# Optimization experiments

Hardware: AMD Instinct MI355X
Metric: run time of the kernel (lower is better)

The kernel has to match this reference:

```python
import jax, jax.numpy as jnp
import numpy as np

T, B, D, R = 1024, 32, 1024, 128

def _orth_cols(key, n, r):
    # mimic torch QR-based orthogonal init: Q[:, :r] of a random [n, r] matrix
    a = jax.random.normal(key, (n, r), dtype=jnp.float32)
    q, _ = jnp.linalg.qr(a)
    return q[:, :r]

def setup_inputs() -> dict:
    key = jax.random.key(0)
    ks = jax.random.split(key, 8)
    x = jax.random.normal(ks[0], (T, B, D), dtype=jnp.float32)
    z = jax.random.normal(ks[1], (T, B, D), dtype=jnp.float32)
    h0 = jnp.zeros((B, D), dtype=jnp.float32)
    U_h = _orth_cols(ks[2], D, R)
    V_h = _orth_cols(ks[3], D, R).T  # [R, D] with orthonormal rows
    U_x = _orth_cols(ks[4], D, R)
    V_x = _orth_cols(ks[5], D, R).T
    s_h = jnp.ones((R,), dtype=jnp.float32)
    s_x = jnp.ones((R,), dtype=jnp.float32)
    b = jnp.zeros((D,), dtype=jnp.float32)
    return {"x": x, "z": z, "h0": h0, "U_h": U_h, "V_h": V_h, "s_h": s_h,
            "U_x": U_x, "V_x": V_x, "s_x": s_x, "b": b}

def reference(x, z, h0, U_h, V_h, s_h, U_x, V_x, s_x, b):
    # Precompute V_x @ x_t for all timesteps: [T, B, R]
    Vx_all = jnp.einsum('tbd,rd->tbr', x, V_x)
    Ux_all = jnp.einsum('tbr,dr->tbd', s_x * Vx_all, U_x)  # input branch, no recurrence

    def step(h_prev, inp):
        Ux_t, z_t = inp
        Vh = h_prev @ V_h.T                 # [B, R]
        Uh = (s_h * Vh) @ U_h.T             # [B, D]
        h_new = jnp.tanh(Uh + Ux_t + b)
        out_t = h_new * jax.nn.silu(z_t)
        return h_new, (h_new, out_t)

    _, (hs, output) = jax.lax.scan(step, h0, (Ux_all, z))
    h = jnp.concatenate([h0[None], hs], axis=0)  # [T+1, B, D]
    return output, h
```

## Files before the change

### kernel.cpp

```cpp
#include <hip/hip_runtime.h>
#include <cstdint>

#define T_STEPS 1024
#define BATCH   32
#define DIM     1024
#define RANK    128
#define BD      (BATCH*DIM)
#define TBD     ((size_t)T_STEPS*BD)

typedef _Float16 half2v __attribute__((ext_vector_type(2)));

__device__ __forceinline__ float dot2f(uint32_t a, uint32_t b, float acc) {
#if __has_builtin(__builtin_amdgcn_fdot2)
  return __builtin_amdgcn_fdot2(__builtin_bit_cast(half2v, a),
                                __builtin_bit_cast(half2v, b), acc, false);
#else
  half2v xx = __builtin_bit_cast(half2v, a);
  half2v yy = __builtin_bit_cast(half2v, b);
  return acc + (float)xx[0]*(float)yy[0] + (float)xx[1]*(float)yy[1];
#endif
}

__device__ __forceinline__ float dot2x4(uint4 w, uint4 h, float acc) {
  acc = dot2f(w.x, h.x, acc); acc = dot2f(w.y, h.y, acc);
  acc = dot2f(w.z, h.z, acc); acc = dot2f(w.w, h.w, acc);
  return acc;
}

__device__ __forceinline__ uint16_t f16b(float x) {
  _Float16 h = (_Float16)x;
  return __builtin_bit_cast(unsigned short, h);
}
__device__ __forceinline__ uint32_t pack2(float a, float b) {
  return (uint32_t)f16b(a) | ((uint32_t)f16b(b) << 16);
}
__device__ __forceinline__ float fast_tanh(float x) {
  float e = __expf(2.0f*x);
  return 1.0f - 2.0f/(e + 1.0f);
}
__device__ __forceinline__ float fast_silu(float zz) {
  return zz / (1.0f + __expf(-zz));
}

template<int K>
__device__ __forceinline__ uint32_t qbcast(uint32_t v) {
  return (uint32_t)__builtin_amdgcn_mov_dpp((int)v, K*0x55, 0xf, 0xf, true);
}
template<int K>
__device__ __forceinline__ uint4 qbcast4(uint4 v) {
  uint4 r;
  r.x = qbcast<K>(v.x); r.y = qbcast<K>(v.y);
  r.z = qbcast<K>(v.z); r.w = qbcast<K>(v.w);
  return r;
}
template<int CTRL>
__device__ __forceinline__ float dpp_xorf(float v) {
  int t = __builtin_amdgcn_mov_dpp(__builtin_bit_cast(int, v), CTRL, 0xf, 0xf, true);
  return __builtin_bit_cast(float, t);
}

__device__ __forceinline__ void lds_barrier() {
  asm volatile("s_waitcnt lgkmcnt(0)" ::: "memory");
  __builtin_amdgcn_s_barrier();
  __builtin_amdgcn_sched_barrier(0);
}

__global__ void prep_kernel(const float* __restrict__ Uh, const float* __restrict__ Vh,
                            const float* __restrict__ sh, const float* __restrict__ Ux,
                            const float* __restrict__ Vx, const float* __restrict__ sx,
                            const float* __restrict__ h0, uint32_t* __restrict__ ws32,
                            float* __restrict__ hout) {
  int i = blockIdx.x*blockDim.x + threadIdx.x;
  int n = gridDim.x*blockDim.x;
  for (int p = i; p < 65536; p += n) {
    int r = p >> 9, dp = p & 511;
    ws32[p] = pack2(Vh[r*1024 + 2*dp], Vh[r*1024 + 2*dp + 1]);
  }
  for (int p = i; p < 65536; p += n) {
    int d = p >> 6, k = p & 63;
    ws32[65536 + p] = pack2(Uh[d*128 + k]      * sh[k],
                            Uh[d*128 + 64 + k] * sh[64 + k]);
  }
  for (int p = i; p < 65536; p += n) {
    int r = p >> 9, dp = p & 511;
    ws32[131072 + p] = pack2(Vx[r*1024 + 2*dp], Vx[r*1024 + 2*dp + 1]);
  }
  for (int p = i; p < 65536; p += n) {
    int d = p >> 6, rp = p & 63;
    ws32[196608 + p] = pack2(Ux[d*128 + 2*rp]   * sx[2*rp],
                             Ux[d*128 + 2*rp+1] * sx[2*rp+1]);
  }
  for (int p = i; p < BD; p += n) hout[p] = h0[p];
}

__global__ __launch_bounds__(512, 4) void inp_kernel(
    const float* __restrict__ x, const uint32_t* __restrict__ ws32,
    const float* __restrict__ bias, float* __restrict__ hout) {
  const int t = blockIdx.x;
  const int l = threadIdx.x;
  __shared__ __attribute__((aligned(16))) uint32_t xs[32*516];
  __shared__ __attribute__((aligned(16))) uint16_t svx[BATCH*RANK];

  const float4* xg = (const float4*)(x + (size_t)t*BD);
  #pragma unroll
  for (int k = 0; k < 16; k++) {
    int i = l + 512*k;
    float4 v = xg[i];
    int bb = i >> 8;
    int d4 = i & 255;
    xs[bb*516 + d4*2]     = pack2(v.x, v.y);
    xs[bb*516 + d4*2 + 1] = pack2(v.z, v.w);
  }
  __syncthreads();

  const int q4 = l & 3;
  const int r  = l >> 2;
  const uint4* wrow = (const uint4*)(ws32 + 131072 + r*512);
  float acc0[8], acc1[8];
  #pragma unroll
  for (int bi = 0; bi < 8; bi++) { acc0[bi] = 0.f; acc1[bi] = 0.f; }
  #pragma unroll 4
  for (int J = 0; J < 128; J += 2) {
    uint4 w0 = wrow[J];
    uint4 w1 = wrow[J+1];
    #pragma unroll
    for (int bi = 0; bi < 8; bi++) {
      const uint4* xrow = (const uint4*)(xs + (4*bi + q4)*516);
      uint4 h0v = xrow[J];
      acc0[bi] = dot2f(w0.x, h0v.x, acc0[bi]);
      acc0[bi] = dot2f(w0.y, h0v.y, acc0[bi]);
      acc0[bi] = dot2f(w0.z, h0v.z, acc0[bi]);
      acc0[bi] = dot2f(w0.w, h0v.w, acc0[bi]);
      uint4 h1v = xrow[J+1];
      acc1[bi] = dot2f(w1.x, h1v.x, acc1[bi]);
      acc1[bi] = dot2f(w1.y, h1v.y, acc1[bi]);
      acc1[bi] = dot2f(w1.z, h1v.z, acc1[bi]);
      acc1[bi] = dot2f(w1.w, h1v.w, acc1[bi]);
    }
  }
  #pragma unroll
  for (int bi = 0; bi < 8; bi++)
    svx[(4*bi + q4)*RANK + r] = f16b(acc0[bi] + acc1[bi]);
  __syncthreads();

  const uint4* svx4 = (const uint4*)svx;
  float accb[BATCH];
  #pragma unroll 1
  for (int dd = 0; dd < 2; dd++) {
    int d = l + dd*512;
    const uint4* urow = (const uint4*)(ws32 + 196608 + d*64);
    #pragma unroll
    for (int bi = 0; bi < BATCH; bi++) accb[bi] = 0.f;
    #pragma unroll
    for (int RP = 0; RP < 16; RP++) {
      uint4 w = urow[RP];
      #pragma unroll
      for (int bi = 0; bi < BATCH; bi++) {
        uint4 sv = svx4[bi*16 + RP];
        accb[bi] = dot2f(w.x, sv.x, accb[bi]);
        accb[bi] = dot2f(w.y, sv.y, accb[bi]);
        accb[bi] = dot2f(w.z, sv.z, accb[bi]);
        accb[bi] = dot2f(w.w, sv.w, accb[bi]);
      }
    }
    float bv = bias[d];
    float* cslot = hout + (size_t)(t+1)*BD + d;
    #pragma unroll
    for (int bi = 0; bi < BATCH; bi++)
      cslot[(size_t)bi*DIM] = accb[bi] + bv;
  }
}

__global__ __attribute__((amdgpu_flat_work_group_size(512, 512),
                          amdgpu_waves_per_eu(2, 2)))
void rec_kernel(
    const uint32_t* __restrict__ ws32, const float* __restrict__ z,
    float* __restrict__ outb) {
  const int b  = blockIdx.x;
  const int l  = threadIdx.x;
  const int W  = l & 31;
  const int R8 = l >> 5;
  const int m  = l & 3;
  float* hout = outb + TBD;
  const uint4* vhw4 = (const uint4*)ws32;
  const uint4* uhw4 = (const uint4*)(ws32 + 65536);

  __shared__ __attribute__((aligned(16))) uint4    vlds[6144];
  __shared__ __attribute__((aligned(16))) uint4    hbuf[32*5];
  __shared__ __attribute__((aligned(16))) uint32_t svh32[64];

  uint4 vw[5][4];
  #pragma unroll
  for (int r = 0; r < 5; r++) {
    #pragma unroll
    for (int c = 0; c < 4; c++) vw[r][c] = vhw4[(8*R8 + r)*128 + W*4 + c];
  }
  #pragma unroll
  for (int rr = 0; rr < 3; rr++) {
    #pragma unroll
    for (int c = 0; c < 4; c++)
      vlds[R8*384 + rr*128 + c*32 + W] = vhw4[(8*R8 + 5 + rr)*128 + W*4 + c];
  }
  uint4 uqr0[16], uqr1[16];
  #pragma unroll
  for (int J = 0; J < 16; J++) { uqr0[J] = uhw4[(2*l)*16 + J]; uqr1[J] = uhw4[(2*l+1)*16 + J]; }
  {
    const float2 v = ((const float2*)(hout + (size_t)b*DIM))[l];
    ((uint32_t*)hbuf)[20*(l>>4) + (l&15)] = pack2(v.x, v.y);
  }
  __syncthreads();

  const float2* zp2 = (const float2*)(z + (size_t)b*DIM) + l;
  float2*       cp2 = (float2*)(hout + BD + (size_t)b*DIM) + l;
  float2*       op2 = (float2*)(outb + (size_t)b*DIM) + l;
  const uint4*  hb4  = hbuf + W*5;
  const uint4*  svh4 = (const uint4*)svh32;
  const int vbase = R8*384;

  #pragma unroll 1
  for (int t = 0; t < T_STEPS; t++) {
    float2 cc = *cp2;
    float2 zz = *zp2;

    float a[8] = {0.f,0.f,0.f,0.f,0.f,0.f,0.f,0.f};
    #pragma unroll
    for (int c = 0; c < 4; c++) {
      uint4 hvc = hb4[c];
      uint4 vA = vlds[vbase + c*32 + W];
      uint4 vB = vlds[vbase + 128 + c*32 + W];
      uint4 vC = vlds[vbase + 256 + c*32 + W];
      a[0] = dot2x4(vw[0][c], hvc, a[0]);
      a[1] = dot2x4(vw[1][c], hvc, a[1]);
      a[2] = dot2x4(vw[2][c], hvc, a[2]);
      a[3] = dot2x4(vw[3][c], hvc, a[3]);
      a[4] = dot2x4(vw[4][c], hvc, a[4]);
      a[5] = dot2x4(vA, hvc, a[5]);
      a[6] = dot2x4(vB, hvc, a[6]);
      a[7] = dot2x4(vC, hvc, a[7]);
    }
    float b4[4];
    {
      const bool s0 = (W & 1);
      #pragma unroll
      for (int i = 0; i < 4; i++) {
        float keep = s0 ? a[2*i+1] : a[2*i];
        float send = s0 ? a[2*i]   : a[2*i+1];
        b4[i] = keep + dpp_xorf<0xB1>(send);
      }
    }
    float c2[2];
    {
      const bool s1 = (W >> 1) & 1;
      #pragma unroll
      for (int i = 0; i < 2; i++) {
        float keep = s1 ? b4[2*i+1] : b4[2*i];
        float send = s1 ? b4[2*i]   : b4[2*i+1];
        c2[i] = keep + dpp_xorf<0x4E>(send);
      }
    }
    float s;
    {
      const bool s2 = (W >> 2) & 1;
      float keep = s2 ? c2[1] : c2[0];
      float send = s2 ? c2[0] : c2[1];
      s = keep + __shfl_xor(send, 4);
    }
    s += __shfl_xor(s, 8);
    s += __shfl_xor(s, 16);
    if (W < 8) {
      int row = 8*R8 + W;
      int idx = ((row & 63) << 1) | (row >> 6);
      ((uint16_t*)svh32)[idx] = f16b(s);
    }
    lds_barrier();

    float p0 = 0.f, p1 = 0.f;
    {
      uint4 svm = svh4[m];
      uint4 sv;
      sv = qbcast4<0>(svm); p0 = dot2x4(uqr0[0], sv, p0); p1 = dot2x4(uqr1[0], sv, p1);
      sv = qbcast4<1>(svm); p0 = dot2x4(uqr0[1], sv, p0); p1 = dot2x4(uqr1[1], sv, p1);
      sv = qbcast4<2>(svm); p0 = dot2x4(uqr0[2], sv, p0); p1 = dot2x4(uqr1[2], sv, p1);
      sv = qbcast4<3>(svm); p0 = dot2x4(uqr0[3], sv, p0); p1 = dot2x4(uqr1[3], sv, p1);
    }
    {
      uint4 svm = svh4[4 + m];
      uint4 sv;
      sv = qbcast4<0>(svm); p0 = dot2x4(uqr0[4], sv, p0); p1 = dot2x4(uqr1[4], sv, p1);
      sv = qbcast4<1>(svm); p0 = dot2x4(uqr0[5], sv, p0); p1 = dot2x4(uqr1[5], sv, p1);
      sv = qbcast4<2>(svm); p0 = dot2x4(uqr0[6], sv, p0); p1 = dot2x4(uqr1[6], sv, p1);
      sv = qbcast4<3>(svm); p0 = dot2x4(uqr0[7], sv, p0); p1 = dot2x4(uqr1[7], sv, p1);
    }
    {
      uint4 svm = svh4[8 + m];
      uint4 sv;
      sv = qbcast4<0>(svm); p0 = dot2x4(uqr0[8],  sv, p0); p1 = dot2x4(uqr1[8],  sv, p1);
      sv = qbcast4<1>(svm); p0 = dot2x4(uqr0[9],  sv, p0); p1 = dot2x4(uqr1[9],  sv, p1);
      sv = qbcast4<2>(svm); p0 = dot2x4(uqr0[10], sv, p0); p1 = dot2x4(uqr1[10], sv, p1);
      sv = qbcast4<3>(svm); p0 = dot2x4(uqr0[11], sv, p0); p1 = dot2x4(uqr1[11], sv, p1);
    }
    {
      uint4 svm = svh4[12 + m];
      uint4 sv;
      sv = qbcast4<0>(svm); p0 = dot2x4(uqr0[12], sv, p0); p1 = dot2x4(uqr1[12], sv, p1);
      sv = qbcast4<1>(svm); p0 = dot2x4(uqr0[13], sv, p0); p1 = dot2x4(uqr1[13], sv, p1);
      sv = qbcast4<2>(svm); p0 = dot2x4(uqr0[14], sv, p0); p1 = dot2x4(uqr1[14], sv, p1);
      sv = qbcast4<3>(svm); p0 = dot2x4(uqr0[15], sv, p0); p1 = dot2x4(uqr1[15], sv, p1);
    }

    float hv0 = fast_tanh(p0 + cc.x);
    float hv1 = fast_tanh(p1 + cc.y);
    *cp2 = make_float2(hv0, hv1);
    ((uint32_t*)hbuf)[20*(l>>4) + (l&15)] = pack2(hv0, hv1);
    *op2 = make_float2(hv0 * fast_silu(zz.x), hv1 * fast_silu(zz.y));
    lds_barrier();

    cp2 += BD/2; zp2 += BD/2; op2 += BD/2;
  }
}

extern "C" void kernel_launch(void* const* d_in, const int* in_sizes, int n_in,
                              void* d_out, int out_size, void* d_ws, size_t ws_size,
                              hipStream_t stream) {
  const float* x  = (const float*)d_in[0];
  const float* z  = (const float*)d_in[1];
  const float* h0 = (const float*)d_in[2];
  const float* Uh = (const float*)d_in[3];
  const float* Vh = (const float*)d_in[4];
  const float* sh = (const float*)d_in[5];
  const float* Ux = (const float*)d_in[6];
  const float* Vx = (const float*)d_in[7];
  const float* sx = (const float*)d_in[8];
  const float* bb = (const float*)d_in[9];
  float* outb = (float*)d_out;
  uint32_t* ws32 = (uint32_t*)d_ws;

  prep_kernel<<<512, 256, 0, stream>>>(Uh, Vh, sh, Ux, Vx, sx, h0, ws32, outb + TBD);
  inp_kernel<<<T_STEPS, 512, 0, stream>>>(x, ws32, bb, outb + TBD);
  rec_kernel<<<BATCH, 512, 0, stream>>>(ws32, z, outb);
}
```

Measured before the change: 2.441 ms.

## Split each batch row's recurrence across two workgroups with global-memory flag exchange

The recurrent kernel now launches 64 workgroups of 256 threads instead of 32 of 512. Each pair handles half of the hidden dimension for one batch row. Partial V_h projections are exchanged every step through workspace buffers, using release/acquire atomic flags and a spin-wait. This spreads the serial recurrence over twice as many CUs and keeps all V_h weights in registers. In exchange it adds a cross-CU handshake on every timestep, whose latency may dominate. It also relies on both partner workgroups being co-resident, or the spin-wait deadlocks.

New measurement: 6.713 ms. 2.75x slower.

```diff
diff --git a/kernel.cpp b/kernel.cpp
--- a/kernel.cpp
+++ b/kernel.cpp
@@ -7,6 +7,9 @@
 #define RANK    128
 #define BD      (BATCH*DIM)
 #define TBD     ((size_t)T_STEPS*BD)
+
+#define WSP_PBUF 262144
+#define WSP_FLAG (WSP_PBUF + 64*256)
 
 typedef _Float16 half2v __attribute__((ext_vector_type(2)));
 
@@ -91,6 +94,7 @@
                              Ux[d*128 + 2*rp+1] * sx[2*rp+1]);
   }
   for (int p = i; p < BD; p += n) hout[p] = h0[p];
+  for (int p = i; p < 1024; p += n) ws32[WSP_FLAG + p] = 0;
 }
 
 __global__ __launch_bounds__(512, 4) void inp_kernel(
@@ -171,76 +175,78 @@
   }
 }
 
-__global__ __attribute__((amdgpu_flat_work_group_size(512, 512),
-                          amdgpu_waves_per_eu(2, 2)))
-void rec_kernel(
-    const uint32_t* __restrict__ ws32, const float* __restrict__ z,
+__global__ __launch_bounds__(256, 1) void rec_kernel(
+    uint32_t* __restrict__ ws32, const float* __restrict__ z,
     float* __restrict__ outb) {
-  const int b  = blockIdx.x;
-  const int l  = threadIdx.x;
-  const int W  = l & 31;
-  const int R8 = l >> 5;
-  const int m  = l & 3;
+  const int g    = blockIdx.x;
+  const int b    = g & 31;
+  const int half = g >> 5;
+  const int l    = threadIdx.x;
+  const int w    = l & 15;
+  const int R16  = l >> 4;
+  const int m    = l & 3;
   float* hout = outb + TBD;
   const uint4* vhw4 = (const uint4*)ws32;
   const uint4* uhw4 = (const uint4*)(ws32 + 65536);
-
-  __shared__ __attribute__((aligned(16))) uint4    vlds[6144];
-  __shared__ __attribute__((aligned(16))) uint4    hbuf[32*5];
+  float*       pmine = (float*)(ws32 + WSP_PBUF) + g*256;
+  const float* pothr = (const float*)(ws32 + WSP_PBUF) + (g^32)*256;
+  int*       fmine = (int*)(ws32 + WSP_FLAG) + g*16;
+  const int* fothr = (const int*)(ws32 + WSP_FLAG) + (g^32)*16;
+
+  __shared__ __attribute__((aligned(16))) uint4    ulds[16*256];
+  __shared__ __attribute__((aligned(16))) uint32_t hbuf[320];
+  __shared__ __attribute__((aligned(16))) float    pown[128];
   __shared__ __attribute__((aligned(16))) uint32_t svh32[64];
 
-  uint4 vw[5][4];
-  #pragma unroll
-  for (int r = 0; r < 5; r++) {
-    #pragma unroll
-    for (int c = 0; c < 4; c++) vw[r][c] = vhw4[(8*R8 + r)*128 + W*4 + c];
-  }
-  #pragma unroll
-  for (int rr = 0; rr < 3; rr++) {
+  uint4 vw[8][4];
+  #pragma unroll
+  for (int rr = 0; rr < 8; rr++) {
     #pragma unroll
     for (int c = 0; c < 4; c++)
-      vlds[R8*384 + rr*128 + c*32 + W] = vhw4[(8*R8 + 5 + rr)*128 + W*4 + c];
-  }
-  uint4 uqr0[16], uqr1[16];
-  #pragma unroll
-  for (int J = 0; J < 16; J++) { uqr0[J] = uhw4[(2*l)*16 + J]; uqr1[J] = uhw4[(2*l+1)*16 + J]; }
+      vw[rr][c] = vhw4[(8*R16 + rr)*128 + half*64 + 4*w + c];
+  }
+  const int d0 = half*512 + 2*l;
+  uint4 uq0[8], uq1[8];
+  #pragma unroll
+  for (int j = 0; j < 8; j++) { uq0[j] = uhw4[d0*16 + j]; uq1[j] = uhw4[(d0+1)*16 + j]; }
+  #pragma unroll
+  for (int jj = 0; jj < 8; jj++) ulds[jj*256 + l]     = uhw4[d0*16     + 8 + jj];
+  #pragma unroll
+  for (int jj = 0; jj < 8; jj++) ulds[(8+jj)*256 + l] = uhw4[(d0+1)*16 + 8 + jj];
   {
-    const float2 v = ((const float2*)(hout + (size_t)b*DIM))[l];
-    ((uint32_t*)hbuf)[20*(l>>4) + (l&15)] = pack2(v.x, v.y);
+    float2 v = ((const float2*)(hout + (size_t)b*DIM + half*512))[l];
+    hbuf[20*(l>>4) + (l&15)] = pack2(v.x, v.y);
   }
   __syncthreads();
 
-  const float2* zp2 = (const float2*)(z + (size_t)b*DIM) + l;
-  float2*       cp2 = (float2*)(hout + BD + (size_t)b*DIM) + l;
-  float2*       op2 = (float2*)(outb + (size_t)b*DIM) + l;
-  const uint4*  hb4  = hbuf + W*5;
+  const float2* zp2 = (const float2*)(z + (size_t)b*DIM + half*512) + l;
+  float2*       cp2 = (float2*)(hout + BD + (size_t)b*DIM + half*512) + l;
+  float2*       op2 = (float2*)(outb + (size_t)b*DIM + half*512) + l;
+  const uint4*  hb4  = (const uint4*)hbuf;
   const uint4*  svh4 = (const uint4*)svh32;
-  const int vbase = R8*384;
 
   #pragma unroll 1
   for (int t = 0; t < T_STEPS; t++) {
     float2 cc = *cp2;
     float2 zz = *zp2;
+    const int par = t & 1;
 
     float a[8] = {0.f,0.f,0.f,0.f,0.f,0.f,0.f,0.f};
     #pragma unroll
     for (int c = 0; c < 4; c++) {
-      uint4 hvc = hb4[c];
-      uint4 vA = vlds[vbase + c*32 + W];
-      uint4 vB = vlds[vbase + 128 + c*32 + W];
-      uint4 vC = vlds[vbase + 256 + c*32 + W];
-      a[0] = dot2x4(vw[0][c], hvc, a[0]);
-      a[1] = dot2x4(vw[1][c], hvc, a[1]);
-      a[2] = dot2x4(vw[2][c], hvc, a[2]);
-      a[3] = dot2x4(vw[3][c], hvc, a[3]);
-      a[4] = dot2x4(vw[4][c], hvc, a[4]);
-      a[5] = dot2x4(vA, hvc, a[5]);
-      a[6] = dot2x4(vB, hvc, a[6]);
-      a[7] = dot2x4(vC, hvc, a[7]);
+      uint4 hv = hb4[5*w + c];
+      a[0] = dot2x4(vw[0][c], hv, a[0]);
+      a[1] = dot2x4(vw[1][c], hv, a[1]);
+      a[2] = dot2x4(vw[2][c], hv, a[2]);
+      a[3] = dot2x4(vw[3][c], hv, a[3]);
+      a[4] = dot2x4(vw[4][c], hv, a[4]);
+      a[5] = dot2x4(vw[5][c], hv, a[5]);
+      a[6] = dot2x4(vw[6][c], hv, a[6]);
+      a[7] = dot2x4(vw[7][c], hv, a[7]);
     }
     float b4[4];
     {
-      const bool s0 = (W & 1);
+      const bool s0 = (w & 1);
       #pragma unroll
       for (int i = 0; i < 4; i++) {
         float keep = s0 ? a[2*i+1] : a[2*i];
@@ -250,7 +256,7 @@
     }
     float c2[2];
     {
-      const bool s1 = (W >> 1) & 1;
+      const bool s1 = (w >> 1) & 1;
       #pragma unroll
       for (int i = 0; i < 2; i++) {
         float keep = s1 ? b4[2*i+1] : b4[2*i];
@@ -260,58 +266,71 @@
     }
     float s;
     {
-      const bool s2 = (W >> 2) & 1;
+      const bool s2 = (w >> 2) & 1;
       float keep = s2 ? c2[1] : c2[0];
       float send = s2 ? c2[0] : c2[1];
       s = keep + __shfl_xor(send, 4);
     }
     s += __shfl_xor(s, 8);
-    s += __shfl_xor(s, 16);
-    if (W < 8) {
-      int row = 8*R8 + W;
-      int idx = ((row & 63) << 1) | (row >> 6);
-      ((uint16_t*)svh32)[idx] = f16b(s);
+    if (w < 8) {
+      int r = 8*R16 + w;
+      pown[r] = s;
+      __hip_atomic_store(pmine + par*128 + r, s,
+                         __ATOMIC_RELAXED, __HIP_MEMORY_SCOPE_AGENT);
+    }
+    __syncthreads();
+    if (l == 0)
+      __hip_atomic_fetch_add(fmine, 1, __ATOMIC_RELEASE, __HIP_MEMORY_SCOPE_AGENT);
+    while (__hip_atomic_load(fothr, __ATOMIC_ACQUIRE, __HIP_MEMORY_SCOPE_AGENT) < t + 1) { }
+    if (l < 64) {
+      float o0 = __hip_atomic_load(pothr + par*128 + l,      __ATOMIC_RELAXED, __HIP_MEMORY_SCOPE_AGENT);
+      float o1 = __hip_atomic_load(pothr + par*128 + l + 64, __ATOMIC_RELAXED, __HIP_MEMORY_SCOPE_AGENT);
+      svh32[l] = pack2(pown[l] + o0, pown[l + 64] + o1);
     }
     lds_barrier();
 
     float p0 = 0.f, p1 = 0.f;
     {
-      uint4 svm = svh4[m];
-      uint4 sv;
-      sv = qbcast4<0>(svm); p0 = dot2x4(uqr0[0], sv, p0); p1 = dot2x4(uqr1[0], sv, p1);
-      sv = qbcast4<1>(svm); p0 = dot2x4(uqr0[1], sv, p0); p1 = dot2x4(uqr1[1], sv, p1);
-      sv = qbcast4<2>(svm); p0 = dot2x4(uqr0[2], sv, p0); p1 = dot2x4(uqr1[2], sv, p1);
-      sv = qbcast4<3>(svm); p0 = dot2x4(uqr0[3], sv, p0); p1 = dot2x4(uqr1[3], sv, p1);
-    }
-    {
-      uint4 svm = svh4[4 + m];
-      uint4 sv;
-      sv = qbcast4<0>(svm); p0 = dot2x4(uqr0[4], sv, p0); p1 = dot2x4(uqr1[4], sv, p1);
-      sv = qbcast4<1>(svm); p0 = dot2x4(uqr0[5], sv, p0); p1 = dot2x4(uqr1[5], sv, p1);
-      sv = qbcast4<2>(svm); p0 = dot2x4(uqr0[6], sv, p0); p1 = dot2x4(uqr1[6], sv, p1);
-      sv = qbcast4<3>(svm); p0 = dot2x4(uqr0[7], sv, p0); p1 = dot2x4(uqr1[7], sv, p1);
-    }
-    {
-      uint4 svm = svh4[8 + m];
-      uint4 sv;
-      sv = qbcast4<0>(svm); p0 = dot2x4(uqr0[8],  sv, p0); p1 = dot2x4(uqr1[8],  sv, p1);
-      sv = qbcast4<1>(svm); p0 = dot2x4(uqr0[9],  sv, p0); p1 = dot2x4(uqr1[9],  sv, p1);
-      sv = qbcast4<2>(svm); p0 = dot2x4(uqr0[10], sv, p0); p1 = dot2x4(uqr1[10], sv, p1);
-      sv = qbcast4<3>(svm); p0 = dot2x4(uqr0[11], sv, p0); p1 = dot2x4(uqr1[11], sv, p1);
-    }
-    {
-      uint4 svm = svh4[12 + m];
-      uint4 sv;
-      sv = qbcast4<0>(svm); p0 = dot2x4(uqr0[12], sv, p0); p1 = dot2x4(uqr1[12], sv, p1);
-      sv = qbcast4<1>(svm); p0 = dot2x4(uqr0[13], sv, p0); p1 = dot2x4(uqr1[13], sv, p1);
-      sv = qbcast4<2>(svm); p0 = dot2x4(uqr0[14], sv, p0); p1 = dot2x4(uqr1[14], sv, p1);
-      sv = qbcast4<3>(svm); p0 = dot2x4(uqr0[15], sv, p0); p1 = dot2x4(uqr1[15], sv, p1);
+      uint4 svm = svh4[m]; uint4 sv;
+      sv = qbcast4<0>(svm); p0 = dot2x4(uq0[0], sv, p0); p1 = dot2x4(uq1[0], sv, p1);
+      sv = qbcast4<1>(svm); p0 = dot2x4(uq0[1], sv, p0); p1 = dot2x4(uq1[1], sv, p1);
+      sv = qbcast4<2>(svm); p0 = dot2x4(uq0[2], sv, p0); p1 = dot2x4(uq1[2], sv, p1);
+      sv = qbcast4<3>(svm); p0 = dot2x4(uq0[3], sv, p0); p1 = dot2x4(uq1[3], sv, p1);
+    }
+    {
+      uint4 svm = svh4[4 + m]; uint4 sv;
+      sv = qbcast4<0>(svm); p0 = dot2x4(uq0[4], sv, p0); p1 = dot2x4(uq1[4], sv, p1);
+      sv = qbcast4<1>(svm); p0 = dot2x4(uq0[5], sv, p0); p1 = dot2x4(uq1[5], sv, p1);
+      sv = qbcast4<2>(svm); p0 = dot2x4(uq0[6], sv, p0); p1 = dot2x4(uq1[6], sv, p1);
+      sv = qbcast4<3>(svm); p0 = dot2x4(uq0[7], sv, p0); p1 = dot2x4(uq1[7], sv, p1);
+    }
+    {
+      uint4 u00 = ulds[l],        u01 = ulds[256 + l];
+      uint4 u02 = ulds[512 + l],  u03 = ulds[768 + l];
+      uint4 u10 = ulds[2048 + l], u11 = ulds[2304 + l];
+      uint4 u12 = ulds[2560 + l], u13 = ulds[2816 + l];
+      uint4 svm = svh4[8 + m]; uint4 sv;
+      sv = qbcast4<0>(svm); p0 = dot2x4(u00, sv, p0); p1 = dot2x4(u10, sv, p1);
+      sv = qbcast4<1>(svm); p0 = dot2x4(u01, sv, p0); p1 = dot2x4(u11, sv, p1);
+      sv = qbcast4<2>(svm); p0 = dot2x4(u02, sv, p0); p1 = dot2x4(u12, sv, p1);
+      sv = qbcast4<3>(svm); p0 = dot2x4(u03, sv, p0); p1 = dot2x4(u13, sv, p1);
+    }
+    {
+      uint4 u00 = ulds[1024 + l], u01 = ulds[1280 + l];
+      uint4 u02 = ulds[1536 + l], u03 = ulds[1792 + l];
+      uint4 u10 = ulds[3072 + l], u11 = ulds[3328 + l];
+      uint4 u12 = ulds[3584 + l], u13 = ulds[3840 + l];
+      uint4 svm = svh4[12 + m]; uint4 sv;
+      sv = qbcast4<0>(svm); p0 = dot2x4(u00, sv, p0); p1 = dot2x4(u10, sv, p1);
+      sv = qbcast4<1>(svm); p0 = dot2x4(u01, sv, p0); p1 = dot2x4(u11, sv, p1);
+      sv = qbcast4<2>(svm); p0 = dot2x4(u02, sv, p0); p1 = dot2x4(u12, sv, p1);
+      sv = qbcast4<3>(svm); p0 = dot2x4(u03, sv, p0); p1 = dot2x4(u13, sv, p1);
     }
 
     float hv0 = fast_tanh(p0 + cc.x);
     float hv1 = fast_tanh(p1 + cc.y);
     *cp2 = make_float2(hv0, hv1);
-    ((uint32_t*)hbuf)[20*(l>>4) + (l&15)] = pack2(hv0, hv1);
+    hbuf[20*(l>>4) + (l&15)] = pack2(hv0, hv1);
     *op2 = make_float2(hv0 * fast_silu(zz.x), hv1 * fast_silu(zz.y));
     lds_barrier();
 
@@ -337,5 +356,5 @@
 
   prep_kernel<<<512, 256, 0, stream>>>(Uh, Vh, sh, Ux, Vx, sx, h0, ws32, outb + TBD);
   inp_kernel<<<T_STEPS, 512, 0, stream>>>(x, ws32, bb, outb + TBD);
-  rec_kernel<<<BATCH, 512, 0, stream>>>(ws32, z, outb);
-}
+  rec_kernel<<<64, 256, 0, stream>>>(ws32, z, outb);
+}
```

## Stream U_h weights from global/L2 each step instead of holding in registers

Applied to the files above, without the earlier changes.

The prep kernel now lays out the scaled U_h weights in a coalesced per-J-slab layout. The recurrent kernel no longer keeps 32 uint4 U_h fragments in registers. Instead it reloads 26 of them from global memory every timestep and keeps the remaining 6 in a new LDS buffer. An empty asm pin on the V_h register fragments is meant to stop the compiler rematerialising or spilling them. The goal is lower register pressure and fewer spills, paid for with an L2 load of U_h inside the serial time loop every step.

After: 3.320 ms. +36.0%, slower.

```diff
diff --git a/kernel.cpp b/kernel.cpp
--- a/kernel.cpp
+++ b/kernel.cpp
@@ -40,6 +40,10 @@
 }
 __device__ __forceinline__ float fast_silu(float zz) {
   return zz / (1.0f + __expf(-zz));
+}
+
+__device__ __forceinline__ void pin4(uint4 &v) {
+  asm volatile("" : "+v"(v.x), "+v"(v.y), "+v"(v.z), "+v"(v.w));
 }
 
 template<int K>
@@ -78,8 +82,14 @@
   }
   for (int p = i; p < 65536; p += n) {
     int d = p >> 6, k = p & 63;
-    ws32[65536 + p] = pack2(Uh[d*128 + k]      * sh[k],
-                            Uh[d*128 + 64 + k] * sh[64 + k]);
+    uint32_t w = pack2(Uh[d*128 + k]      * sh[k],
+                       Uh[d*128 + 64 + k] * sh[64 + k]);
+    if (k < 52) {
+      int J = (k >> 2) + 13*(d & 1);
+      ws32[65536 + J*2048 + (d >> 1)*4 + (k & 3)] = w;
+    } else {
+      ws32[118784 + d*12 + (k - 52)] = w;
+    }
   }
   for (int p = i; p < 65536; p += n) {
     int r = p >> 9, dp = p & 511;
@@ -183,9 +193,11 @@
   const int m  = l & 3;
   float* hout = outb + TBD;
   const uint4* vhw4 = (const uint4*)ws32;
-  const uint4* uhw4 = (const uint4*)(ws32 + 65536);
+  const uint4* uqs4 = (const uint4*)(ws32 + 65536);
+  const uint4* ures4 = (const uint4*)(ws32 + 118784);
 
   __shared__ __attribute__((aligned(16))) uint4    vlds[6144];
+  __shared__ __attribute__((aligned(16))) uint4    ulds[3072];
   __shared__ __attribute__((aligned(16))) uint4    hbuf[32*5];
   __shared__ __attribute__((aligned(16))) uint32_t svh32[64];
 
@@ -196,14 +208,21 @@
     for (int c = 0; c < 4; c++) vw[r][c] = vhw4[(8*R8 + r)*128 + W*4 + c];
   }
   #pragma unroll
+  for (int r = 0; r < 5; r++) {
+    #pragma unroll
+    for (int c = 0; c < 4; c++) pin4(vw[r][c]);
+  }
+  #pragma unroll
   for (int rr = 0; rr < 3; rr++) {
     #pragma unroll
     for (int c = 0; c < 4; c++)
       vlds[R8*384 + rr*128 + c*32 + W] = vhw4[(8*R8 + 5 + rr)*128 + W*4 + c];
   }
-  uint4 uqr0[16], uqr1[16];
-  #pragma unroll
-  for (int J = 0; J < 16; J++) { uqr0[J] = uhw4[(2*l)*16 + J]; uqr1[J] = uhw4[(2*l+1)*16 + J]; }
+  #pragma unroll
+  for (int j = 0; j < 3; j++) {
+    ulds[j*512 + l]       = ures4[(2*l)*3 + j];
+    ulds[(3+j)*512 + l]   = ures4[(2*l+1)*3 + j];
+  }
   {
     const float2 v = ((const float2*)(hout + (size_t)b*DIM))[l];
     ((uint32_t*)hbuf)[20*(l>>4) + (l&15)] = pack2(v.x, v.y);
@@ -276,36 +295,48 @@
 
     float p0 = 0.f, p1 = 0.f;
     {
-      uint4 svm = svh4[m];
-      uint4 sv;
-      sv = qbcast4<0>(svm); p0 = dot2x4(uqr0[0], sv, p0); p1 = dot2x4(uqr1[0], sv, p1);
-      sv = qbcast4<1>(svm); p0 = dot2x4(uqr0[1], sv, p0); p1 = dot2x4(uqr1[1], sv, p1);
-      sv = qbcast4<2>(svm); p0 = dot2x4(uqr0[2], sv, p0); p1 = dot2x4(uqr1[2], sv, p1);
-      sv = qbcast4<3>(svm); p0 = dot2x4(uqr0[3], sv, p0); p1 = dot2x4(uqr1[3], sv, p1);
-    }
-    {
-      uint4 svm = svh4[4 + m];
-      uint4 sv;
-      sv = qbcast4<0>(svm); p0 = dot2x4(uqr0[4], sv, p0); p1 = dot2x4(uqr1[4], sv, p1);
-      sv = qbcast4<1>(svm); p0 = dot2x4(uqr0[5], sv, p0); p1 = dot2x4(uqr1[5], sv, p1);
-      sv = qbcast4<2>(svm); p0 = dot2x4(uqr0[6], sv, p0); p1 = dot2x4(uqr1[6], sv, p1);
-      sv = qbcast4<3>(svm); p0 = dot2x4(uqr0[7], sv, p0); p1 = dot2x4(uqr1[7], sv, p1);
-    }
-    {
-      uint4 svm = svh4[8 + m];
-      uint4 sv;
-      sv = qbcast4<0>(svm); p0 = dot2x4(uqr0[8],  sv, p0); p1 = dot2x4(uqr1[8],  sv, p1);
-      sv = qbcast4<1>(svm); p0 = dot2x4(uqr0[9],  sv, p0); p1 = dot2x4(uqr1[9],  sv, p1);
-      sv = qbcast4<2>(svm); p0 = dot2x4(uqr0[10], sv, p0); p1 = dot2x4(uqr1[10], sv, p1);
-      sv = qbcast4<3>(svm); p0 = dot2x4(uqr0[11], sv, p0); p1 = dot2x4(uqr1[11], sv, p1);
-    }
-    {
-      uint4 svm = svh4[12 + m];
-      uint4 sv;
-      sv = qbcast4<0>(svm); p0 = dot2x4(uqr0[12], sv, p0); p1 = dot2x4(uqr1[12], sv, p1);
-      sv = qbcast4<1>(svm); p0 = dot2x4(uqr0[13], sv, p0); p1 = dot2x4(uqr1[13], sv, p1);
-      sv = qbcast4<2>(svm); p0 = dot2x4(uqr0[14], sv, p0); p1 = dot2x4(uqr1[14], sv, p1);
-      sv = qbcast4<3>(svm); p0 = dot2x4(uqr0[15], sv, p0); p1 = dot2x4(uqr1[15], sv, p1);
+      uint4 u00 = uqs4[0*512 + l],  u01 = uqs4[1*512 + l],
+            u02 = uqs4[2*512 + l],  u03 = uqs4[3*512 + l];
+      uint4 u10 = uqs4[13*512 + l], u11 = uqs4[14*512 + l],
+            u12 = uqs4[15*512 + l], u13 = uqs4[16*512 + l];
+      uint4 svm = svh4[m]; uint4 sv;
+      sv = qbcast4<0>(svm); p0 = dot2x4(u00, sv, p0); p1 = dot2x4(u10, sv, p1);
+      sv = qbcast4<1>(svm); p0 = dot2x4(u01, sv, p0); p1 = dot2x4(u11, sv, p1);
+      sv = qbcast4<2>(svm); p0 = dot2x4(u02, sv, p0); p1 = dot2x4(u12, sv, p1);
+      sv = qbcast4<3>(svm); p0 = dot2x4(u03, sv, p0); p1 = dot2x4(u13, sv, p1);
+    }
+    {
+      uint4 u00 = uqs4[4*512 + l],  u01 = uqs4[5*512 + l],
+            u02 = uqs4[6*512 + l],  u03 = uqs4[7*512 + l];
+      uint4 u10 = uqs4[17*512 + l], u11 = uqs4[18*512 + l],
+            u12 = uqs4[19*512 + l], u13 = uqs4[20*512 + l];
+      uint4 svm = svh4[4 + m]; uint4 sv;
+      sv = qbcast4<0>(svm); p0 = dot2x4(u00, sv, p0); p1 = dot2x4(u10, sv, p1);
+      sv = qbcast4<1>(svm); p0 = dot2x4(u01, sv, p0); p1 = dot2x4(u11, sv, p1);
+      sv = qbcast4<2>(svm); p0 = dot2x4(u02, sv, p0); p1 = dot2x4(u12, sv, p1);
+      sv = qbcast4<3>(svm); p0 = dot2x4(u03, sv, p0); p1 = dot2x4(u13, sv, p1);
+    }
+    {
+      uint4 u00 = uqs4[8*512 + l],  u01 = uqs4[9*512 + l],
+            u02 = uqs4[10*512 + l], u03 = uqs4[11*512 + l];
+      uint4 u10 = uqs4[21*512 + l], u11 = uqs4[22*512 + l],
+            u12 = uqs4[23*512 + l], u13 = uqs4[24*512 + l];
+      uint4 svm = svh4[8 + m]; uint4 sv;
+      sv = qbcast4<0>(svm); p0 = dot2x4(u00, sv, p0); p1 = dot2x4(u10, sv, p1);
+      sv = qbcast4<1>(svm); p0 = dot2x4(u01, sv, p0); p1 = dot2x4(u11, sv, p1);
+      sv = qbcast4<2>(svm); p0 = dot2x4(u02, sv, p0); p1 = dot2x4(u12, sv, p1);
+      sv = qbcast4<3>(svm); p0 = dot2x4(u03, sv, p0); p1 = dot2x4(u13, sv, p1);
+    }
+    {
+      uint4 u0a = uqs4[12*512 + l];
+      uint4 u1a = uqs4[25*512 + l];
+      uint4 u0b = ulds[0*512 + l], u0c = ulds[1*512 + l], u0d = ulds[2*512 + l];
+      uint4 u1b = ulds[3*512 + l], u1c = ulds[4*512 + l], u1d = ulds[5*512 + l];
+      uint4 svm = svh4[12 + m]; uint4 sv;
+      sv = qbcast4<0>(svm); p0 = dot2x4(u0a, sv, p0); p1 = dot2x4(u1a, sv, p1);
+      sv = qbcast4<1>(svm); p0 = dot2x4(u0b, sv, p0); p1 = dot2x4(u1b, sv, p1);
+      sv = qbcast4<2>(svm); p0 = dot2x4(u0c, sv, p0); p1 = dot2x4(u1c, sv, p1);
+      sv = qbcast4<3>(svm); p0 = dot2x4(u0d, sv, p0); p1 = dot2x4(u1d, sv, p1);
     }
 
     float hv0 = fast_tanh(p0 + cc.x);
```
